# Kernel tuning notes

Hardware: AMD Instinct MI355X
Metric: run time of the kernel (lower is better)

## Reference

```python
import jax, jax.numpy as jnp
from jax import lax
import numpy as np

VOCAB = 2048
EMB = 256
LAT = 128
MAX_SENLEN = 8
SIZE_LAT = 3.0
BATCH = 32


def lm_softmax(tokens, E, Wi, Wh, b):
    """Embedding(mask_zero) -> LSTM(units=VOCAB) -> softmax. tokens: [B, L] int."""
    B, L = tokens.shape
    emb = E[tokens]                      # [B, L, EMB]
    mask = (tokens != 0)                 # PAD==0 is masked (Keras mask_zero)
    H = Wh.shape[0]

    def step(carry, xm):
        h, c = carry
        x, m = xm                        # x: [B, EMB], m: [B]
        gates = x @ Wi + h @ Wh + b      # [B, 4H], Keras gate order i,f,g,o
        i, f, g, o = jnp.split(gates, 4, axis=1)
        i = jax.nn.sigmoid(i)
        f = jax.nn.sigmoid(f)
        g = jnp.tanh(g)
        o = jax.nn.sigmoid(o)
        c_new = f * c + i * g
        h_new = o * jnp.tanh(c_new)
        m = m[:, None]
        h = jnp.where(m, h_new, h)       # masked steps carry state through
        c = jnp.where(m, c_new, c)
        return (h, c), None

    h0 = jnp.zeros((B, H), emb.dtype)
    (h, _), _ = lax.scan(step, (h0, h0), (jnp.swapaxes(emb, 0, 1), mask.T))
    return jax.nn.softmax(h, axis=-1)    # [B, VOCAB]


def setup_inputs() -> dict:
    key = jax.random.key(0)
    k1, k2, k3, k4 = jax.random.split(key, 4)
    input_tokens = jax.random.randint(k1, (BATCH, MAX_SENLEN), 0, VOCAB, dtype=jnp.int32)
    E = jax.random.normal(k2, (VOCAB, EMB), jnp.float32) * 0.02
    Wi = jax.random.normal(k3, (EMB, 4 * VOCAB), jnp.float32) * 0.02
    Wh = jax.random.normal(k4, (VOCAB, 4 * VOCAB), jnp.float32) * 0.02
    b = jnp.zeros((4 * VOCAB,), jnp.float32).at[VOCAB:2 * VOCAB].set(1.0)  # unit_forget_bias
    return {"input_tokens": input_tokens, "E": E, "Wi": Wi, "Wh": Wh, "b": b}


def reference(input_tokens, E, Wi, Wh, b):
    """Unrolled DAriEL_Encoder_Cell_2 RNN: returns z sequence [B, T, LAT]."""
    B, T = input_tokens.shape
    tokens = jnp.zeros((B, T + 1), jnp.int32)        # tokens state, col 0 = PAD
    # RNN zero initial state: bounds both zero at t=0 (cond keeps them since timeStep==0)
    low = jnp.zeros((B, LAT), jnp.float32)
    upp = jnp.zeros((B, LAT), jnp.float32)
    outs = []
    for t in range(T):
        # replace_column(tokens, input_token, timeStep+1)
        tokens = tokens.at[:, t + 1].set(input_tokens[:, t])
        if t > 0:  # tf.cond(mean(timeStep) > 0, initial bounds, state bounds)
            low = jnp.zeros((B, LAT), jnp.float32)
            upp = jnp.full((B, LAT), SIZE_LAT, jnp.float32)
        sm = lm_softmax(tokens[:, : t + 1], E, Wi, Wh, b)   # LM on prefix s_0toj
        s_j = tokens[:, t + 1]                               # current token
        c_inc = jnp.cumsum(sm, axis=1)
        c_exc = c_inc - sm
        cu = jnp.take_along_axis(c_inc, s_j[:, None], axis=1)  # [B,1]
        cl = jnp.take_along_axis(c_exc, s_j[:, None], axis=1)  # [B,1]
        rng = upp - low
        new_low = low + rng * cl
        upp = low + rng * cu
        low = new_low
        z = (low + upp) * 0.5            # mean over stacked bounds
        outs.append(z)
    return jnp.stack(outs, axis=1)       # [B, T, LAT]
```

## Files before the change

kernel.cpp:

```cpp
#include <hip/hip_runtime.h>

#define BATCH 32
#define TT 8
#define VOCAB 2048
#define EMB 256
#define NG 8192
#define LAT 128
#define KTOT 2304
#define NKT 72
#define NNT 512
#define NJT 128

#define WSCALE 4096.0f
#define ASCALE 16.0f
#define DQ (1.0f/65536.0f)

typedef float f32x4 __attribute__((ext_vector_type(4)));

#define EAC_OFF 0
#define FLG_OFF 256
#define ZP_OFF  4352
#define SP_OFF  33024
#define AFX_OFF 61696
#define AFH_OFF 76032
#define BP_OFF  108800

#define AT_LD(p)    __hip_atomic_load((p),  __ATOMIC_RELAXED, __HIP_MEMORY_SCOPE_AGENT)
#define AT_ST(p,v)  __hip_atomic_store((p), (v), __ATOMIC_RELAXED, __HIP_MEMORY_SCOPE_AGENT)

__device__ __forceinline__ float sigmoidf_(float x){ return 1.f/(1.f+__expf(-x)); }
__device__ __forceinline__ float tanhf_(float x){
  x = fminf(fmaxf(x, -10.f), 10.f);
  float e = __expf(2.f*x);
  return (e-1.f)/(e+1.f);
}
__device__ __forceinline__ unsigned char f2e4m3(float f){
  const unsigned int u = __float_as_uint(f);
  const unsigned int sign = (u >> 24) & 0x80u;
  const unsigned int au = u & 0x7FFFFFFFu;
  const unsigned int r = au + 0x0007FFFFu + ((au >> 20) & 1u);
  unsigned int code = (((r >> 23) - 120u) << 3) | ((r >> 20) & 7u);
  code = (code > 0x7Eu) ? 0x7Eu : code;
  const float a = __uint_as_float(au);
  const unsigned int sub = (unsigned int)rintf(a * 512.0f);
  code = (au < 0x3C800000u) ? sub : code;
  return (unsigned char)(sign | code);
}

__global__ __launch_bounds__(256) void k_pack(
    const int* __restrict__ tok, const float* __restrict__ E,
    const float* __restrict__ Wi, const float* __restrict__ Wh,
    unsigned long long* __restrict__ Bp,
    unsigned long long* __restrict__ AfX, unsigned long long* __restrict__ AfH1,
    int* __restrict__ flg, float* __restrict__ out){
  const int tid = threadIdx.x;
  const int nb = blockIdx.x;
  const int kt = blockIdx.y;
  __shared__ unsigned char lds[32][64];
  {
    const int kl = tid >> 3;
    const int n0 = (tid & 7) * 8;
    const int k  = kt*32 + kl;
    const float* W = (k < EMB) ? (Wi + (size_t)k*NG) : (Wh + (size_t)(k-EMB)*NG);
    const float4 f0 = *(const float4*)(W + nb*64 + n0);
    const float4 f1 = *(const float4*)(W + nb*64 + n0 + 4);
    unsigned long long pk = 0ull;
    pk |= (unsigned long long)f2e4m3(f0.x*WSCALE);
    pk |= (unsigned long long)f2e4m3(f0.y*WSCALE) << 8;
    pk |= (unsigned long long)f2e4m3(f0.z*WSCALE) << 16;
    pk |= (unsigned long long)f2e4m3(f0.w*WSCALE) << 24;
    pk |= (unsigned long long)f2e4m3(f1.x*WSCALE) << 32;
    pk |= (unsigned long long)f2e4m3(f1.y*WSCALE) << 40;
    pk |= (unsigned long long)f2e4m3(f1.z*WSCALE) << 48;
    pk |= (unsigned long long)f2e4m3(f1.w*WSCALE) << 56;
    *(unsigned long long*)&lds[kl][n0] = pk;
  }
  __syncthreads();
  {
    const int ntl = tid >> 6, lane = tid & 63;
    const int kgrp = lane >> 4, n16 = lane & 15;
    unsigned long long pk = 0ull;
    #pragma unroll
    for (int p=0;p<8;p++)
      pk |= ((unsigned long long)lds[kgrp*8 + p][ntl*16 + n16]) << (8*p);
    Bp[((size_t)(nb*4 + ntl)*NKT + kt)*64 + lane] = pk;
  }
  const int i = (kt*128 + nb)*256 + tid;
  if (i < 7*32*32){
    const int s   = i >> 10;
    const int rem = i & 1023;
    const int b   = rem >> 5;
    const int kgi = rem & 31;
    const int tk  = tok[b*TT + s];
    const float4 e0 = *(const float4*)(E + (size_t)tk*EMB + kgi*8);
    const float4 e1 = *(const float4*)(E + (size_t)tk*EMB + kgi*8 + 4);
    unsigned long long pk = 0ull;
    pk |= (unsigned long long)f2e4m3(e0.x*ASCALE);
    pk |= (unsigned long long)f2e4m3(e0.y*ASCALE) << 8;
    pk |= (unsigned long long)f2e4m3(e0.z*ASCALE) << 16;
    pk |= (unsigned long long)f2e4m3(e0.w*ASCALE) << 24;
    pk |= (unsigned long long)f2e4m3(e1.x*ASCALE) << 32;
    pk |= (unsigned long long)f2e4m3(e1.y*ASCALE) << 40;
    pk |= (unsigned long long)f2e4m3(e1.z*ASCALE) << 48;
    pk |= (unsigned long long)f2e4m3(e1.w*ASCALE) << 56;
    AfX[((size_t)((s*2 + (b>>4))*8 + (kgi>>2)))*64 + (kgi&3)*16 + (b&15)] = pk;
  }
  if (i < 8192) AfH1[i] = 0ull;
  if (i < BATCH*LAT)
    out[(size_t)((i>>7)*TT + 0)*LAT + (i&(LAT-1))] = 0.f;
  if (i < 4096) flg[i] = 0;
}

__global__ __launch_bounds__(256, 1) void k_fused(
    const int* __restrict__ tok, const float* __restrict__ bias,
    float* __restrict__ out, float* __restrict__ Zp, float* __restrict__ Sp,
    float* __restrict__ Eac, const unsigned long long* __restrict__ AfX,
    unsigned long long* __restrict__ AfH, const unsigned long long* __restrict__ Bp,
    int* __restrict__ flg){
  const int tid = threadIdx.x;
  const int bid = blockIdx.x;
  const int jt = bid & 127, mh = bid >> 7;
  const int g = tid >> 6, lane = tid & 63;
  const int quad = lane >> 4, col = lane & 15;

  __shared__ float gsh[4][16][16];
  __shared__ long hlds[64][64];
  __shared__ unsigned char hsh[256];
  __shared__ float zsh[2];

  const long* __restrict__ BpV = (const long*)Bp;
  const size_t bbase = (size_t)(g*NJT + jt)*NKT*64 + lane;
  long Breg[NKT];
  #pragma unroll
  for (int i=0;i<NKT;i++) Breg[i] = BpV[bbase + (size_t)i*64];
  #pragma unroll
  for (int i=0;i<NKT;i++) asm volatile("" : "+v"(Breg[i]));

  const int b16 = tid >> 4, jj = tid & 15;
  const int b = mh*16 + b16;
  const int j = jt*16 + jj;
  const float bi  = bias[j];
  const float bff = bias[j + VOCAB];
  const float bgg = bias[j + 2*VOCAB];
  const float boo = bias[j + 3*VOCAB];
  const int hoff = ((jj>>3)&1)*128 + b16*8 + (jj&7);
  const size_t bofs = (size_t)(mh*64 + (jt>>1))*512 + (size_t)(jt&1)*256;
  float hreg = 0.f, creg = 0.f;

  for (int t=1; t<TT; t++){
    const long* __restrict__ aX = (const long*)AfX + (size_t)((t-1)*2 + mh)*512 + lane;
    f32x4 acc = {0,0,0,0};
    #pragma unroll
    for (int kt=0; kt<8; kt++)
      acc = __builtin_amdgcn_mfma_f32_16x16x32_fp8_fp8(aX[(size_t)kt*64], Breg[kt], acc, 0,0,0);

    if (t >= 2){
      const int want = t-1;
      if (tid < 64){
        for (;;){
          int done = 1;
          #pragma unroll
          for (int q2=0;q2<4;q2++)
            done &= (AT_LD(&flg[(tid*4+q2)*16]) >= want) ? 1 : 0;
          if (done) break;
          __builtin_amdgcn_s_sleep(2);
        }
      }
      asm volatile("" ::: "memory");
    }
    __syncthreads();

    {
      unsigned long long* aH = AfH + (size_t)(t&1)*8192 + (size_t)mh*4096;
      long hl[16];
      #pragma unroll
      for (int i=0;i<16;i++)
        hl[i] = (long)AT_LD(&aH[(size_t)(g*16+i)*64 + lane]);
      #pragma unroll
      for (int i=0;i<16;i++) hlds[g*16+i][lane] = hl[i];
    }
    __syncthreads();

    #pragma unroll
    for (int kt=8; kt<NKT; kt++)
      acc = __builtin_amdgcn_mfma_f32_16x16x32_fp8_fp8(hlds[kt-8][lane], Breg[kt], acc, 0,0,0);
    #pragma unroll
    for (int r=0;r<4;r++) gsh[g][quad*4 + r][col] = acc[r];
    __syncthreads();

    const float ip = gsh[0][b16][jj]*DQ + bi;
    const float fp = gsh[1][b16][jj]*DQ + bff;
    const float gg = gsh[2][b16][jj]*DQ + bgg;
    const float op = gsh[3][b16][jj]*DQ + boo;
    const float cn = sigmoidf_(fp)*creg + sigmoidf_(ip)*tanhf_(gg);
    const float hn = sigmoidf_(op)*tanhf_(cn);
    if (tok[b*TT + (t-1)] != 0){ hreg = hn; creg = cn; }
    hsh[hoff] = f2e4m3(ASCALE*hreg);
    const int sj = tok[b*TT + t];
    const float e = __expf(hreg);
    if (j == sj) AT_ST(&Eac[(t-1)*32 + b], e);
    float z = e, s = (j < sj) ? e : 0.f;
    #pragma unroll
    for (int m=1; m<16; m<<=1){ z += __shfl_xor(z, m); s += __shfl_xor(s, m); }
    if (jj == 0){
      AT_ST(&Zp[((size_t)(t-1)*32 + b)*128 + jt], z);
      AT_ST(&Sp[((size_t)(t-1)*32 + b)*128 + jt], s);
    }
    __syncthreads();

    if (tid < 32){
      unsigned long long* dst =
        (unsigned long long*)((unsigned char*)AfH + (size_t)((t&1)^1)*65536 + bofs);
      AT_ST(&dst[tid], ((const unsigned long long*)hsh)[tid]);
    }
    asm volatile("s_waitcnt vmcnt(0)" ::: "memory");
    __syncthreads();
    if (tid == 0) AT_ST(&flg[bid*16], t);

    if (t >= 2 && bid < BATCH){
      const int s = t-2;
      if (tid < 64){
        float zl = AT_LD(&Zp[((size_t)s*32+bid)*128 + tid])
                 + AT_LD(&Zp[((size_t)s*32+bid)*128 + tid + 64]);
        float sl = AT_LD(&Sp[((size_t)s*32+bid)*128 + tid])
                 + AT_LD(&Sp[((size_t)s*32+bid)*128 + tid + 64]);
        #pragma unroll
        for (int m=1; m<64; m<<=1){ zl += __shfl_xor(zl, m); sl += __shfl_xor(sl, m); }
        if (tid == 0){ zsh[0] = zl; zsh[1] = sl; }
      }
      __syncthreads();
      if (tid < LAT){
        const float Ej = AT_LD(&Eac[s*32 + bid]);
        out[((size_t)bid*TT + (t-1))*LAT + tid] = (3.f*zsh[1] + 1.5f*Ej)/zsh[0];
      }
    }
  }

  if (bid < BATCH){
    while (AT_LD(&flg[tid*16]) < TT-1) __builtin_amdgcn_s_sleep(1);
    asm volatile("" ::: "memory");
    __syncthreads();
    const int s = TT-2;
    if (tid < 64){
      float zl = AT_LD(&Zp[((size_t)s*32+bid)*128 + tid])
               + AT_LD(&Zp[((size_t)s*32+bid)*128 + tid + 64]);
      float sl = AT_LD(&Sp[((size_t)s*32+bid)*128 + tid])
               + AT_LD(&Sp[((size_t)s*32+bid)*128 + tid + 64]);
      #pragma unroll
      for (int m=1; m<64; m<<=1){ zl += __shfl_xor(zl, m); sl += __shfl_xor(sl, m); }
      if (tid == 0){ zsh[0] = zl; zsh[1] = sl; }
    }
    __syncthreads();
    if (tid < LAT){
      const float Ej = AT_LD(&Eac[s*32 + bid]);
      out[((size_t)bid*TT + (TT-1))*LAT + tid] = (3.f*zsh[1] + 1.5f*Ej)/zsh[0];
    }
  }
}

extern "C" void kernel_launch(void* const* d_in, const int* in_sizes, int n_in,
                              void* d_out, int out_size, void* d_ws, size_t ws_size,
                              hipStream_t stream){
  const int*   tok  = (const int*)d_in[0];
  const float* E    = (const float*)d_in[1];
  const float* Wi   = (const float*)d_in[2];
  const float* Wh   = (const float*)d_in[3];
  const float* bias = (const float*)d_in[4];
  float* out = (float*)d_out;
  float* ws  = (float*)d_ws;
  float* Eac = ws + EAC_OFF;
  int*   flg = (int*)(ws + FLG_OFF);
  float* Zp  = ws + ZP_OFF;
  float* Sp  = ws + SP_OFF;
  unsigned long long* AfX = (unsigned long long*)(ws + AFX_OFF);
  unsigned long long* AfH = (unsigned long long*)(ws + AFH_OFF);
  unsigned long long* Bp  = (unsigned long long*)(ws + BP_OFF);

  k_pack<<<dim3(128, NKT), 256, 0, stream>>>(tok, E, Wi, Wh, Bp, AfX, AfH + 8192,
                                             flg, out);
  k_fused<<<256, 256, 0, stream>>>(tok, bias, out, Zp, Sp, Eac, AfX, AfH, Bp, flg);
}
```

Before: 141.6 us.

## Move per-step output finalization after the recurrence, spread across 224 blocks

```diff
diff --git a/kernel.cpp b/kernel.cpp
--- a/kernel.cpp
+++ b/kernel.cpp
@@ -163,7 +163,7 @@
           for (int q2=0;q2<4;q2++)
             done &= (AT_LD(&flg[(tid*4+q2)*16]) >= want) ? 1 : 0;
           if (done) break;
-          __builtin_amdgcn_s_sleep(2);
+          __builtin_amdgcn_s_sleep(1);
         }
       }
       asm volatile("" ::: "memory");
@@ -216,44 +216,35 @@
     asm volatile("s_waitcnt vmcnt(0)" ::: "memory");
     __syncthreads();
     if (tid == 0) AT_ST(&flg[bid*16], t);
-
-    if (t >= 2 && bid < BATCH){
-      const int s = t-2;
-      if (tid < 64){
-        float zl = AT_LD(&Zp[((size_t)s*32+bid)*128 + tid])
-                 + AT_LD(&Zp[((size_t)s*32+bid)*128 + tid + 64]);
-        float sl = AT_LD(&Sp[((size_t)s*32+bid)*128 + tid])
-                 + AT_LD(&Sp[((size_t)s*32+bid)*128 + tid + 64]);
+  }
+
+  if (bid < 7*BATCH){
+    const int s = bid >> 5, b2 = bid & 31;
+    if (tid < 64){
+      for (;;){
+        int done = 1;
         #pragma unroll
-        for (int m=1; m<64; m<<=1){ zl += __shfl_xor(zl, m); sl += __shfl_xor(sl, m); }
-        if (tid == 0){ zsh[0] = zl; zsh[1] = sl; }
+        for (int q2=0;q2<4;q2++)
+          done &= (AT_LD(&flg[(tid*4+q2)*16]) >= TT-1) ? 1 : 0;
+        if (done) break;
+        __builtin_amdgcn_s_sleep(1);
       }
-      __syncthreads();
-      if (tid < LAT){
-        const float Ej = AT_LD(&Eac[s*32 + bid]);
-        out[((size_t)bid*TT + (t-1))*LAT + tid] = (3.f*zsh[1] + 1.5f*Ej)/zsh[0];
-      }
-    }
-  }
-
-  if (bid < BATCH){
-    while (AT_LD(&flg[tid*16]) < TT-1) __builtin_amdgcn_s_sleep(1);
+    }
     asm volatile("" ::: "memory");
     __syncthreads();
-    const int s = TT-2;
     if (tid < 64){
-      float zl = AT_LD(&Zp[((size_t)s*32+bid)*128 + tid])
-               + AT_LD(&Zp[((size_t)s*32+bid)*128 + tid + 64]);
-      float sl = AT_LD(&Sp[((size_t)s*32+bid)*128 + tid])
-               + AT_LD(&Sp[((size_t)s*32+bid)*128 + tid + 64]);
+      float zl = AT_LD(&Zp[((size_t)s*32+b2)*128 + tid])
+               + AT_LD(&Zp[((size_t)s*32+b2)*128 + tid + 64]);
+      float sl = AT_LD(&Sp[((size_t)s*32+b2)*128 + tid])
+               + AT_LD(&Sp[((size_t)s*32+b2)*128 + tid + 64]);
       #pragma unroll
       for (int m=1; m<64; m<<=1){ zl += __shfl_xor(zl, m); sl += __shfl_xor(sl, m); }
       if (tid == 0){ zsh[0] = zl; zsh[1] = sl; }
     }
     __syncthreads();
     if (tid < LAT){
-      const float Ej = AT_LD(&Eac[s*32 + bid]);
-      out[((size_t)bid*TT + (TT-1))*LAT + tid] = (3.f*zsh[1] + 1.5f*Ej)/zsh[0];
+      const float Ej = AT_LD(&Eac[s*32 + b2]);
+      out[((size_t)b2*TT + (s+1))*LAT + tid] = (3.f*zsh[1] + 1.5f*Ej)/zsh[0];
     }
   }
 }
```

New measurement: 139.6 us. No clear change (-1.4%).
